# Optimization experiments

Hardware: AMD Instinct MI355X
Metric: run time of the kernel (lower is better)

The kernel has to match this reference:

```python
import jax, jax.numpy as jnp
import numpy as np

H = 512

def setup_inputs() -> dict:
    key = jax.random.key(0)
    ks = jax.random.split(key, 8)
    b, s, m, n, h = 8, 128, 32, 64, H
    sc = 1.0 / np.sqrt(h)
    return {
        "x": jax.random.normal(ks[0], (b, s, m, h), dtype=jnp.float32),
        "y": jax.random.normal(ks[1], (b, s, n, h), dtype=jnp.float32),
        # MultiHeadSelfAtt (additive self-attentive pooling: b*m*h -> b*h)
        "Wa1": jax.random.normal(ks[2], (h, h), dtype=jnp.float32) * sc,
        "ba1": jnp.zeros((h,), dtype=jnp.float32),
        "wa2": jax.random.normal(ks[3], (h,), dtype=jnp.float32) * sc,
        # gate Linear(2h -> h), torch layout weight: (h, 2h)
        "Wl": jax.random.normal(ks[4], (h, 2 * h), dtype=jnp.float32) * (1.0 / np.sqrt(2 * h)),
        "bl": jnp.zeros((h,), dtype=jnp.float32),
    }

def reference(x, y, Wa1, ba1, wa2, Wl, bl):
    h = x.shape[-1]
    # attentive pooling over m for every (b, s) slice: b s m h -> b s h
    scores = jnp.tanh(x @ Wa1 + ba1) @ wa2          # b s m
    attn = jax.nn.softmax(scores, axis=-1)
    pooled = jnp.einsum('bsm,bsmh->bsh', attn, x)   # b s h
    # step i (i>=1) uses pooled x at step i-1
    i_x = pooled[:, :-1]                            # b (s-1) h
    Wy, Wi = Wl[:, :h], Wl[:, h:]                   # split concat-linear
    pre = jnp.einsum('bsnh,gh->bsng', y[:, 1:], Wy) \
        + (i_x @ Wi.T + bl)[:, :, None, :]          # b (s-1) n h
    gate = jax.nn.sigmoid(pre)
    out_rest = y[:, 1:] + i_x[:, :, None, :] * gate
    return jnp.concatenate([y[:, :1], out_rest], axis=1)  # b s n h
```

## Files before the change

kernel.cpp:

```cpp
#include <hip/hip_runtime.h>
#include <cstdint>
#include <cstddef>

#define H 512
#define SEQ 128

typedef __bf16 v8bf __attribute__((ext_vector_type(8)));
typedef float v4f __attribute__((ext_vector_type(4)));
typedef unsigned short v8us __attribute__((ext_vector_type(8)));

__device__ __forceinline__ unsigned short f2bf(float f) {
    unsigned int u = __float_as_uint(f);
    u = (u + 0x7FFFu + ((u >> 16) & 1u)) >> 16;
    return (unsigned short)u;
}
__device__ __forceinline__ float bf2f(unsigned short h) {
    return __uint_as_float(((unsigned int)h) << 16);
}
__device__ __forceinline__ v8bf load_bf8(const unsigned short* p) {
    return *reinterpret_cast<const v8bf*>(p);
}
__device__ __forceinline__ float fast_tanh(float v) {
    float e = __expf(2.f * v);
    return 1.f - 2.f * __builtin_amdgcn_rcpf(e + 1.f);
}
__device__ __forceinline__ float fast_sigmoid(float v) {
    return __builtin_amdgcn_rcpf(1.f + __expf(-v));
}
__device__ __forceinline__ v8us cvt8u(float4 lo, float4 hi) {
    v8us r;
    r[0] = f2bf(lo.x); r[1] = f2bf(lo.y); r[2] = f2bf(lo.z); r[3] = f2bf(lo.w);
    r[4] = f2bf(hi.x); r[5] = f2bf(hi.y); r[6] = f2bf(hi.z); r[7] = f2bf(hi.w);
    return r;
}


__global__ __launch_bounds__(256) void prep_kernel(
        const float* __restrict__ Wa1, const float* __restrict__ Wl,
        unsigned short* __restrict__ WyS, unsigned short* __restrict__ WiS,
        unsigned short* __restrict__ WaS) {
    int tg = blockIdx.x * 256 + threadIdx.x;
    int mat = tg >> 15;
    int idx = tg & 32767;
    int lane = idx & 63;
    int ks = (idx >> 6) & 15;
    int c = idx >> 10;
    int g = c * 16 + (lane & 15);
    int hb = ks * 32 + ((lane >> 4) << 3);
    unsigned short o[8];
    unsigned short* dst;
    if (mat == 0) {
        const float* s = Wl + (size_t)g * 1024 + hb;
#pragma unroll
        for (int j = 0; j < 8; ++j) o[j] = f2bf(s[j]);
        dst = WyS + (size_t)idx * 8;
    } else if (mat == 1) {
        const float* s = Wl + (size_t)g * 1024 + 512 + hb;
#pragma unroll
        for (int j = 0; j < 8; ++j) o[j] = f2bf(s[j]);
        dst = WiS + (size_t)idx * 8;
    } else {
#pragma unroll
        for (int j = 0; j < 8; ++j) o[j] = f2bf(Wa1[(size_t)(hb + j) * H + g]);
        dst = WaS + (size_t)idx * 8;
    }
    *reinterpret_cast<ushort4*>(dst)     = *reinterpret_cast<ushort4*>(&o[0]);
    *reinterpret_cast<ushort4*>(dst + 4) = *reinterpret_cast<ushort4*>(&o[4]);
}

__global__ __launch_bounds__(256, 4) void attn_pool_kernel(
        const float* __restrict__ x, const unsigned short* __restrict__ WaS,
        const float* __restrict__ ba1, const float* __restrict__ wa2,
        float* __restrict__ ixf, unsigned short* __restrict__ ixb) {
    __shared__ __align__(16) unsigned short Xb[32][520];
    __shared__ float attn[32];
    __shared__ float scpart[4][32];

    int bid = blockIdx.x;
    int b = bid / 127, s = bid % 127;
    int t = threadIdx.x;

    const float4* x4 = reinterpret_cast<const float4*>(x + (size_t)(b * SEQ + s) * 32 * H);
#pragma unroll
    for (int i = 0; i < 16; ++i) {
        int idx4 = t + i * 256;
        float4 v = x4[idx4];
        int e = idx4 * 4, m = e >> 9, h = e & 511;
        ushort4 o;
        o.x = f2bf(v.x); o.y = f2bf(v.y); o.z = f2bf(v.z); o.w = f2bf(v.w);
        *reinterpret_cast<ushort4*>(&Xb[m][h]) = o;
    }
    __syncthreads();

    int w = t >> 6, lane = t & 63, q = lane >> 4, c16 = lane & 15;

    v4f acc[2][8];
#pragma unroll
    for (int mi = 0; mi < 2; ++mi)
#pragma unroll
        for (int ci = 0; ci < 8; ++ci) acc[mi][ci] = (v4f){0.f, 0.f, 0.f, 0.f};

    const unsigned short* Bb = WaS + (size_t)(w * 8 * 16) * 512 + lane * 8;

#pragma unroll
    for (int ks = 0; ks < 16; ++ks) {
        v8bf a0 = load_bf8(&Xb[c16][ks * 32 + q * 8]);
        v8bf a1 = load_bf8(&Xb[16 + c16][ks * 32 + q * 8]);
#pragma unroll
        for (int ci = 0; ci < 8; ++ci) {
            v8bf bb = load_bf8(Bb + (size_t)(ci * 16 + ks) * 512);
            acc[0][ci] = __builtin_amdgcn_mfma_f32_16x16x32_bf16(a0, bb, acc[0][ci], 0, 0, 0);
            acc[1][ci] = __builtin_amdgcn_mfma_f32_16x16x32_bf16(a1, bb, acc[1][ci], 0, 0, 0);
        }
    }

    float sr[2][4] = {{0.f, 0.f, 0.f, 0.f}, {0.f, 0.f, 0.f, 0.f}};
#pragma unroll
    for (int ci = 0; ci < 8; ++ci) {
        int g = (w * 8 + ci) * 16 + c16;
        float w2 = wa2[g];
        float bv = ba1[g];
#pragma unroll
        for (int mi = 0; mi < 2; ++mi)
#pragma unroll
            for (int i = 0; i < 4; ++i)
                sr[mi][i] += w2 * fast_tanh(acc[mi][ci][i] + bv);
    }
#pragma unroll
    for (int off = 1; off < 16; off <<= 1) {
#pragma unroll
        for (int mi = 0; mi < 2; ++mi)
#pragma unroll
            for (int i = 0; i < 4; ++i) sr[mi][i] += __shfl_xor(sr[mi][i], off);
    }
    if (c16 == 0) {
#pragma unroll
        for (int mi = 0; mi < 2; ++mi)
#pragma unroll
            for (int i = 0; i < 4; ++i) scpart[w][mi * 16 + q * 4 + i] = sr[mi][i];
    }
    __syncthreads();

    if (t < 64) {
        int m = t & 31;
        float v = scpart[0][m] + scpart[1][m] + scpart[2][m] + scpart[3][m];
        float mx = v;
#pragma unroll
        for (int off = 1; off < 32; off <<= 1) mx = fmaxf(mx, __shfl_xor(mx, off));
        float e = __expf(v - mx);
        float sum = e;
#pragma unroll
        for (int off = 1; off < 32; off <<= 1) sum += __shfl_xor(sum, off);
        if (t < 32) attn[m] = e * __builtin_amdgcn_rcpf(sum);
    }
    __syncthreads();

    int h0 = t * 2;
    float p0 = 0.f, p1 = 0.f;
#pragma unroll
    for (int m = 0; m < 32; ++m) {
        float am = attn[m];
        p0 += am * bf2f(Xb[m][h0]);
        p1 += am * bf2f(Xb[m][h0 + 1]);
    }
    size_t r = (size_t)bid;
    ixf[r * H + h0] = p0;
    ixf[r * H + h0 + 1] = p1;
    ixb[r * H + h0] = f2bf(p0);
    ixb[r * H + h0 + 1] = f2bf(p1);
}

__global__ __launch_bounds__(256) void ipre_kernel(
        const unsigned short* __restrict__ ixb, const unsigned short* __restrict__ WiS,
        const float* __restrict__ bl, float* __restrict__ ipre) {
    int row16 = blockIdx.x * 16;
    int t = threadIdx.x, w = t >> 6, lane = t & 63, q = lane >> 4, c16 = lane & 15;
    int c0 = blockIdx.y * 8 + w * 2;

    v4f acc0 = {0.f, 0.f, 0.f, 0.f};
    v4f acc1 = {0.f, 0.f, 0.f, 0.f};
    const unsigned short* arow = ixb + (size_t)(row16 + c16) * H + q * 8;
#pragma unroll
    for (int ks = 0; ks < 16; ++ks) {
        v8bf a = load_bf8(arow + ks * 32);
        acc0 = __builtin_amdgcn_mfma_f32_16x16x32_bf16(
            a, load_bf8(WiS + (size_t)(c0 * 16 + ks) * 512 + lane * 8), acc0, 0, 0, 0);
        acc1 = __builtin_amdgcn_mfma_f32_16x16x32_bf16(
            a, load_bf8(WiS + (size_t)((c0 + 1) * 16 + ks) * 512 + lane * 8), acc1, 0, 0, 0);
    }
#pragma unroll
    for (int cc = 0; cc < 2; ++cc) {
        int g = (c0 + cc) * 16 + c16;
        float blv = bl[g];
        v4f a = cc ? acc1 : acc0;
#pragma unroll
        for (int i = 0; i < 4; ++i) {
            int row = row16 + q * 4 + i;
            if (row < 1016) ipre[(size_t)row * H + g] = a[i] + blv;
        }
    }
}

__global__ __launch_bounds__(512, 4) void main_kernel(
        const float* __restrict__ y, const unsigned short* __restrict__ WyS,
        const float* __restrict__ ixf, const float* __restrict__ ipre,
        float* __restrict__ out) {
    int bid = blockIdx.x;
    int t = threadIdx.x;

    if (bid >= 1016) {
        int cb = bid - 1016;
        int b = cb >> 1, half = cb & 1;
        size_t base = ((size_t)(b * SEQ)) * 64 * H + (size_t)half * 32 * H;
        const float4* y4 = reinterpret_cast<const float4*>(y + base);
        float4* o4 = reinterpret_cast<float4*>(out + base);
#pragma unroll
        for (int i = 0; i < 8; ++i) o4[t + i * 512] = y4[t + i * 512];
        return;
    }

    int rg = bid >> 1;
    int ch = bid & 1;

    __shared__ __align__(16) char arena[57344];
    unsigned short* Ab = (unsigned short*)arena;
    unsigned short* Bbuf = (unsigned short*)(arena + 20480);
    float* ip_s = (float*)(arena + 53248);
    float* ix_s = (float*)(arena + 55296);
    float* ep   = (float*)arena;

    int t0 = rg * 2;

    int arow  = t >> 2;
    int acol0 = (t & 3) * 8;
    int atid  = t0 + (arow >> 6);
    int ab    = atid / 127, asm1 = atid % 127;
    const float* yrow = y + ((size_t)(ab * SEQ + asm1 + 1) * 64 + (arow & 63)) * H;

    int w = t >> 6, lane = t & 63, q = lane >> 4, c16 = lane & 15;
    int ck0 = w * 2;
    const unsigned short* bsrc0 = WyS + (size_t)((ch * 16 + ck0) * 16) * 512 + lane * 8;
    const unsigned short* bsrc1 = WyS + (size_t)((ch * 16 + ck0 + 1) * 16) * 512 + lane * 8;

    {
        int tile = t >> 8, gl = t & 255;
        size_t rrow = (size_t)(t0 + tile) * H + ch * 256 + gl;
        ip_s[t] = ipre[rrow];
        ix_s[t] = ixf[rrow];
    }

    {
        float4 a0 = *reinterpret_cast<const float4*>(yrow + acol0);
        float4 a1 = *reinterpret_cast<const float4*>(yrow + acol0 + 4);
        v8us b0 = *reinterpret_cast<const v8us*>(bsrc0);
        v8us b1 = *reinterpret_cast<const v8us*>(bsrc1);
        *reinterpret_cast<v8us*>(&Ab[arow * 40 + acol0]) = cvt8u(a0, a1);
        *reinterpret_cast<v8us*>(&Bbuf[ck0 * 512 + lane * 8]) = b0;
        *reinterpret_cast<v8us*>(&Bbuf[(ck0 + 1) * 512 + lane * 8]) = b1;
    }
    __syncthreads();

    int wr = w >> 1;
    int wc = w & 1;

    v4f acc[2][8];
#pragma unroll
    for (int rt = 0; rt < 2; ++rt)
#pragma unroll
        for (int ci = 0; ci < 8; ++ci) acc[rt][ci] = (v4f){0.f, 0.f, 0.f, 0.f};

#pragma unroll
    for (int p = 0; p < 16; ++p) {
        const int cur = p & 1;
        float4 na0, na1; v8us nb0, nb1;
        if (p < 15) {
            na0 = *reinterpret_cast<const float4*>(yrow + (p + 1) * 32 + acol0);
            na1 = *reinterpret_cast<const float4*>(yrow + (p + 1) * 32 + acol0 + 4);
            nb0 = *reinterpret_cast<const v8us*>(bsrc0 + (p + 1) * 512);
            nb1 = *reinterpret_cast<const v8us*>(bsrc1 + (p + 1) * 512);
        }

        v8bf af0 = load_bf8(&Ab[cur * 5120 + (wr * 32 + c16) * 40 + q * 8]);
        v8bf af1 = load_bf8(&Ab[cur * 5120 + (wr * 32 + 16 + c16) * 40 + q * 8]);
#pragma unroll
        for (int ci = 0; ci < 8; ++ci) {
            v8bf bf = load_bf8(&Bbuf[cur * 8192 + (wc * 8 + ci) * 512 + lane * 8]);
            acc[0][ci] = __builtin_amdgcn_mfma_f32_16x16x32_bf16(af0, bf, acc[0][ci], 0, 0, 0);
            acc[1][ci] = __builtin_amdgcn_mfma_f32_16x16x32_bf16(af1, bf, acc[1][ci], 0, 0, 0);
        }

        if (p < 15) {
            *reinterpret_cast<v8us*>(&Ab[(cur ^ 1) * 5120 + arow * 40 + acol0]) = cvt8u(na0, na1);
            *reinterpret_cast<v8us*>(&Bbuf[(cur ^ 1) * 8192 + ck0 * 512 + lane * 8]) = nb0;
            *reinterpret_cast<v8us*>(&Bbuf[(cur ^ 1) * 8192 + (ck0 + 1) * 512 + lane * 8]) = nb1;
            __syncthreads();
        }
    }

    int tile = wr >> 1;
    size_t obase0 = ((size_t)((t0 / 127) * SEQ + t0 % 127 + 1) * 64) * H;
    size_t obase1 = ((size_t)(((t0 + 1) / 127) * SEQ + (t0 + 1) % 127 + 1) * 64) * H;

#pragma unroll
    for (int slab = 0; slab < 4; ++slab) {
        __syncthreads();
        if (wr == slab) {
#pragma unroll
            for (int ci = 0; ci < 8; ++ci) {
                int gl = wc * 128 + ci * 16 + c16;
                float ip = ip_s[tile * 256 + gl];
                float ixv = ix_s[tile * 256 + gl];
#pragma unroll
                for (int rt = 0; rt < 2; ++rt)
#pragma unroll
                    for (int i = 0; i < 4; ++i) {
                        int rl = rt * 16 + q * 4 + i;
                        ep[rl * 260 + gl] = ixv * fast_sigmoid(acc[rt][ci][i] + ip);
                    }
            }
        }
        __syncthreads();
#pragma unroll
        for (int k = 0; k < 4; ++k) {
            int c = t + k * 512;
            int rl = c >> 6;
            int cx = (c & 63) * 4;
            int browg = slab * 32 + rl;
            int tl = browg >> 6;
            int n = browg & 63;
            size_t off = (tl ? obase1 : obase0) + (size_t)n * H + ch * 256 + cx;
            float4 g4 = *reinterpret_cast<const float4*>(&ep[rl * 260 + cx]);
            float4 y4 = *reinterpret_cast<const float4*>(&y[off]);
            float4 o;
            o.x = y4.x + g4.x; o.y = y4.y + g4.y;
            o.z = y4.z + g4.z; o.w = y4.w + g4.w;
            *reinterpret_cast<float4*>(&out[off]) = o;
        }
    }
}

extern "C" void kernel_launch(void* const* d_in, const int* in_sizes, int n_in,
                              void* d_out, int out_size, void* d_ws, size_t ws_size,
                              hipStream_t stream) {
    const float* x   = (const float*)d_in[0];
    const float* y   = (const float*)d_in[1];
    const float* Wa1 = (const float*)d_in[2];
    const float* ba1 = (const float*)d_in[3];
    const float* wa2 = (const float*)d_in[4];
    const float* Wl  = (const float*)d_in[5];
    const float* bl  = (const float*)d_in[6];
    float* out = (float*)d_out;

    char* ws = (char*)d_ws;
    unsigned short* WyS  = (unsigned short*)(ws);
    unsigned short* WiS  = (unsigned short*)(ws + 524288);
    unsigned short* WaS  = (unsigned short*)(ws + 1048576);
    float*          ixf  = (float*)(ws + 1572864);
    unsigned short* ixb  = (unsigned short*)(ws + 3670016);
    float*          ipre = (float*)(ws + 4718592);

    hipLaunchKernelGGL(prep_kernel, dim3(384), dim3(256), 0, stream, Wa1, Wl, WyS, WiS, WaS);
    hipLaunchKernelGGL(attn_pool_kernel, dim3(1016), dim3(256), 0, stream,
                       x, WaS, ba1, wa2, ixf, ixb);
    hipLaunchKernelGGL(ipre_kernel, dim3(64, 4), dim3(256), 0, stream, ixb, WiS, bl, ipre);
    hipLaunchKernelGGL(main_kernel, dim3(1032), dim3(512), 0, stream,
                       y, WyS, ixf, ipre, out);
}
```

Before: 150.9 us.

## Shrink main GEMM tile to one timestep, async-load weights into LDS, swizzle blocks

Restructures the main gated GEMM so each 256-thread block handles one (b,s) slice of 64 rows instead of two, doubling the grid to 2048 blocks and cutting LDS use. Weight tiles now go straight from global memory into LDS with global_load_lds, and the y activations are prefetched two stages ahead in registers so loads overlap the MFMA loop better. Block IDs are remapped with an XCD-style swizzle to improve L2 locality. The aim is more blocks resident per CU and better latency hiding, at the cost of each block reusing its weight tile across fewer rows, so weight traffic per output increases.

```diff
diff --git a/kernel.cpp b/kernel.cpp
--- a/kernel.cpp
+++ b/kernel.cpp
@@ -32,6 +32,11 @@
     r[0] = f2bf(lo.x); r[1] = f2bf(lo.y); r[2] = f2bf(lo.z); r[3] = f2bf(lo.w);
     r[4] = f2bf(hi.x); r[5] = f2bf(hi.y); r[6] = f2bf(hi.z); r[7] = f2bf(hi.w);
     return r;
+}
+__device__ __forceinline__ void gll16(const unsigned short* g, unsigned short* l) {
+    __builtin_amdgcn_global_load_lds(
+        (const __attribute__((address_space(1))) unsigned int*)g,
+        (__attribute__((address_space(3))) unsigned int*)l, 16, 0, 0);
 }
 
 
@@ -201,68 +206,64 @@
     }
 }
 
-__global__ __launch_bounds__(512, 4) void main_kernel(
+__global__ __launch_bounds__(256, 3) void main_kernel(
         const float* __restrict__ y, const unsigned short* __restrict__ WyS,
         const float* __restrict__ ixf, const float* __restrict__ ipre,
         float* __restrict__ out) {
-    int bid = blockIdx.x;
+    int bid0 = blockIdx.x;
     int t = threadIdx.x;
 
-    if (bid >= 1016) {
-        int cb = bid - 1016;
+    if (bid0 >= 2032) {
+        int cb = bid0 - 2032;
         int b = cb >> 1, half = cb & 1;
         size_t base = ((size_t)(b * SEQ)) * 64 * H + (size_t)half * 32 * H;
         const float4* y4 = reinterpret_cast<const float4*>(y + base);
         float4* o4 = reinterpret_cast<float4*>(out + base);
 #pragma unroll
-        for (int i = 0; i < 8; ++i) o4[t + i * 512] = y4[t + i * 512];
+        for (int i = 0; i < 16; ++i) o4[t + i * 256] = y4[t + i * 256];
         return;
     }
 
+    int bid = (bid0 & 7) * 254 + (bid0 >> 3);
     int rg = bid >> 1;
     int ch = bid & 1;
 
-    __shared__ __align__(16) char arena[57344];
-    unsigned short* Ab = (unsigned short*)arena;
-    unsigned short* Bbuf = (unsigned short*)(arena + 20480);
-    float* ip_s = (float*)(arena + 53248);
-    float* ix_s = (float*)(arena + 55296);
+    __shared__ __align__(16) char arena[45056];
+    unsigned short* As = (unsigned short*)arena;
+    unsigned short* Bs = (unsigned short*)(arena + 10240);
+    float* ip_s = (float*)(arena + 43008);
+    float* ix_s = (float*)(arena + 44032);
     float* ep   = (float*)arena;
 
-    int t0 = rg * 2;
-
-    int arow  = t >> 2;
-    int acol0 = (t & 3) * 8;
-    int atid  = t0 + (arow >> 6);
-    int ab    = atid / 127, asm1 = atid % 127;
-    const float* yrow = y + ((size_t)(ab * SEQ + asm1 + 1) * 64 + (arow & 63)) * H;
+    int b0 = rg / 127, s0 = rg % 127;
+    size_t obase = ((size_t)(b0 * SEQ + s0 + 1) * 64) * H;
 
     int w = t >> 6, lane = t & 63, q = lane >> 4, c16 = lane & 15;
-    int ck0 = w * 2;
-    const unsigned short* bsrc0 = WyS + (size_t)((ch * 16 + ck0) * 16) * 512 + lane * 8;
-    const unsigned short* bsrc1 = WyS + (size_t)((ch * 16 + ck0 + 1) * 16) * 512 + lane * 8;
+    int wr = w >> 1, wc = w & 1;
+
+    int arow = t >> 2;
+    int acol = (t & 3) * 8;
+    const float* ysrc = y + obase + (size_t)arow * H + acol;
+
+    const unsigned short* bbase = WyS + ((size_t)((ch * 16 + w * 4) * 16)) * 512 + lane * 8;
 
     {
-        int tile = t >> 8, gl = t & 255;
-        size_t rrow = (size_t)(t0 + tile) * H + ch * 256 + gl;
-        ip_s[t] = ipre[rrow];
-        ix_s[t] = ixf[rrow];
-    }
-
-    {
-        float4 a0 = *reinterpret_cast<const float4*>(yrow + acol0);
-        float4 a1 = *reinterpret_cast<const float4*>(yrow + acol0 + 4);
-        v8us b0 = *reinterpret_cast<const v8us*>(bsrc0);
-        v8us b1 = *reinterpret_cast<const v8us*>(bsrc1);
-        *reinterpret_cast<v8us*>(&Ab[arow * 40 + acol0]) = cvt8u(a0, a1);
-        *reinterpret_cast<v8us*>(&Bbuf[ck0 * 512 + lane * 8]) = b0;
-        *reinterpret_cast<v8us*>(&Bbuf[(ck0 + 1) * 512 + lane * 8]) = b1;
-    }
+        size_t rr = (size_t)rg * H + ch * 256 + t;
+        ip_s[t] = ipre[rr];
+        ix_s[t] = ixf[rr];
+    }
+
+#pragma unroll
+    for (int j = 0; j < 4; ++j)
+        gll16(bbase + (size_t)j * 8192, &Bs[(w * 4 + j) * 512]);
+    float4 alo[2], ahi[2];
+    alo[0] = *reinterpret_cast<const float4*>(ysrc);
+    ahi[0] = *reinterpret_cast<const float4*>(ysrc + 4);
+    alo[1] = *reinterpret_cast<const float4*>(ysrc + 32);
+    ahi[1] = *reinterpret_cast<const float4*>(ysrc + 36);
+    *reinterpret_cast<v8us*>(&As[arow * 40 + acol]) = cvt8u(alo[0], ahi[0]);
     __syncthreads();
 
-    int wr = w >> 1;
-    int wc = w & 1;
-
     v4f acc[2][8];
 #pragma unroll
     for (int rt = 0; rt < 2; ++rt)
@@ -271,69 +272,66 @@
 
 #pragma unroll
     for (int p = 0; p < 16; ++p) {
-        const int cur = p & 1;
-        float4 na0, na1; v8us nb0, nb1;
+        const int buf = p & 1;
+        const int nxt = buf ^ 1;
         if (p < 15) {
-            na0 = *reinterpret_cast<const float4*>(yrow + (p + 1) * 32 + acol0);
-            na1 = *reinterpret_cast<const float4*>(yrow + (p + 1) * 32 + acol0 + 4);
-            nb0 = *reinterpret_cast<const v8us*>(bsrc0 + (p + 1) * 512);
-            nb1 = *reinterpret_cast<const v8us*>(bsrc1 + (p + 1) * 512);
-        }
-
-        v8bf af0 = load_bf8(&Ab[cur * 5120 + (wr * 32 + c16) * 40 + q * 8]);
-        v8bf af1 = load_bf8(&Ab[cur * 5120 + (wr * 32 + 16 + c16) * 40 + q * 8]);
+#pragma unroll
+            for (int j = 0; j < 4; ++j)
+                gll16(bbase + (size_t)j * 8192 + (size_t)(p + 1) * 512,
+                      &Bs[nxt * 8192 + (w * 4 + j) * 512]);
+        }
+        if (p < 14) {
+            alo[buf] = *reinterpret_cast<const float4*>(ysrc + (p + 2) * 32);
+            ahi[buf] = *reinterpret_cast<const float4*>(ysrc + (p + 2) * 32 + 4);
+        }
+        if (p < 15) {
+            *reinterpret_cast<v8us*>(&As[nxt * 2560 + arow * 40 + acol]) =
+                cvt8u(alo[nxt], ahi[nxt]);
+        }
+
+        v8bf af0 = load_bf8(&As[buf * 2560 + (wr * 32 + c16) * 40 + q * 8]);
+        v8bf af1 = load_bf8(&As[buf * 2560 + (wr * 32 + 16 + c16) * 40 + q * 8]);
 #pragma unroll
         for (int ci = 0; ci < 8; ++ci) {
-            v8bf bf = load_bf8(&Bbuf[cur * 8192 + (wc * 8 + ci) * 512 + lane * 8]);
-            acc[0][ci] = __builtin_amdgcn_mfma_f32_16x16x32_bf16(af0, bf, acc[0][ci], 0, 0, 0);
-            acc[1][ci] = __builtin_amdgcn_mfma_f32_16x16x32_bf16(af1, bf, acc[1][ci], 0, 0, 0);
-        }
-
-        if (p < 15) {
-            *reinterpret_cast<v8us*>(&Ab[(cur ^ 1) * 5120 + arow * 40 + acol0]) = cvt8u(na0, na1);
-            *reinterpret_cast<v8us*>(&Bbuf[(cur ^ 1) * 8192 + ck0 * 512 + lane * 8]) = nb0;
-            *reinterpret_cast<v8us*>(&Bbuf[(cur ^ 1) * 8192 + (ck0 + 1) * 512 + lane * 8]) = nb1;
-            __syncthreads();
-        }
-    }
-
-    int tile = wr >> 1;
-    size_t obase0 = ((size_t)((t0 / 127) * SEQ + t0 % 127 + 1) * 64) * H;
-    size_t obase1 = ((size_t)(((t0 + 1) / 127) * SEQ + (t0 + 1) % 127 + 1) * 64) * H;
-
-#pragma unroll
-    for (int slab = 0; slab < 4; ++slab) {
+            v8bf bfc = load_bf8(&Bs[buf * 8192 + (wc * 8 + ci) * 512 + lane * 8]);
+            acc[0][ci] = __builtin_amdgcn_mfma_f32_16x16x32_bf16(af0, bfc, acc[0][ci], 0, 0, 0);
+            acc[1][ci] = __builtin_amdgcn_mfma_f32_16x16x32_bf16(af1, bfc, acc[1][ci], 0, 0, 0);
+        }
+
+        if (p < 15) __syncthreads();
+    }
+
+#pragma unroll
+    for (int s = 0; s < 2; ++s) {
         __syncthreads();
-        if (wr == slab) {
+        if (wr == s) {
 #pragma unroll
             for (int ci = 0; ci < 8; ++ci) {
                 int gl = wc * 128 + ci * 16 + c16;
-                float ip = ip_s[tile * 256 + gl];
-                float ixv = ix_s[tile * 256 + gl];
+                float ipv = ip_s[gl];
+                float ixv = ix_s[gl];
 #pragma unroll
                 for (int rt = 0; rt < 2; ++rt)
 #pragma unroll
                     for (int i = 0; i < 4; ++i) {
                         int rl = rt * 16 + q * 4 + i;
-                        ep[rl * 260 + gl] = ixv * fast_sigmoid(acc[rt][ci][i] + ip);
+                        ep[rl * 260 + gl] = ixv * fast_sigmoid(acc[rt][ci][i] + ipv);
                     }
             }
         }
         __syncthreads();
 #pragma unroll
-        for (int k = 0; k < 4; ++k) {
-            int c = t + k * 512;
+        for (int k = 0; k < 8; ++k) {
+            int c = t + k * 256;
             int rl = c >> 6;
             int cx = (c & 63) * 4;
-            int browg = slab * 32 + rl;
-            int tl = browg >> 6;
-            int n = browg & 63;
-            size_t off = (tl ? obase1 : obase0) + (size_t)n * H + ch * 256 + cx;
+            int n = s * 32 + rl;
+            size_t off = obase + (size_t)n * H + ch * 256 + cx;
             float4 g4 = *reinterpret_cast<const float4*>(&ep[rl * 260 + cx]);
-            float4 y4 = *reinterpret_cast<const float4*>(&y[off]);
+            float4 yv = *reinterpret_cast<const float4*>(&y[off]);
             float4 o;
-            o.x = y4.x + g4.x; o.y = y4.y + g4.y;
-            o.z = y4.z + g4.z; o.w = y4.w + g4.w;
+            o.x = yv.x + g4.x; o.y = yv.y + g4.y;
+            o.z = yv.z + g4.z; o.w = yv.w + g4.w;
             *reinterpret_cast<float4*>(&out[off]) = o;
         }
     }
@@ -363,6 +361,6 @@
     hipLaunchKernelGGL(attn_pool_kernel, dim3(1016), dim3(256), 0, stream,
                        x, WaS, ba1, wa2, ixf, ixb);
     hipLaunchKernelGGL(ipre_kernel, dim3(64, 4), dim3(256), 0, stream, ixb, WiS, bl, ipre);
-    hipLaunchKernelGGL(main_kernel, dim3(1032), dim3(512), 0, stream,
+    hipLaunchKernelGGL(main_kernel, dim3(2048), dim3(256), 0, stream,
                        y, WyS, ixf, ipre, out);
 }
```

After: 152.2 us. Within noise of the previous version (+0.9%).

## Prefetch two K-steps ahead in registers and remap block order for XCD locality

Applied to the files above, without the earlier changes.

The GEMM main loop now keeps global loads for the y and Wy tiles two iterations ahead in double-buffered registers. It writes the next stage to shared memory before the MFMAs rather than after, so memory latency can hide behind more compute. Block IDs for the compute blocks are also permuted as (bid&7)*127+(bid>>3), so that consecutive row groups land on the same XCD and can share L2. The cost is higher register pressure from the extra prefetch buffers, under a launch bound of 4 blocks of 512 threads.

```diff
diff --git a/kernel.cpp b/kernel.cpp
--- a/kernel.cpp
+++ b/kernel.cpp
@@ -205,11 +205,11 @@
         const float* __restrict__ y, const unsigned short* __restrict__ WyS,
         const float* __restrict__ ixf, const float* __restrict__ ipre,
         float* __restrict__ out) {
-    int bid = blockIdx.x;
+    int bid0 = blockIdx.x;
     int t = threadIdx.x;
 
-    if (bid >= 1016) {
-        int cb = bid - 1016;
+    if (bid0 >= 1016) {
+        int cb = bid0 - 1016;
         int b = cb >> 1, half = cb & 1;
         size_t base = ((size_t)(b * SEQ)) * 64 * H + (size_t)half * 32 * H;
         const float4* y4 = reinterpret_cast<const float4*>(y + base);
@@ -218,6 +218,8 @@
         for (int i = 0; i < 8; ++i) o4[t + i * 512] = y4[t + i * 512];
         return;
     }
+
+    int bid = (bid0 & 7) * 127 + (bid0 >> 3);
 
     int rg = bid >> 1;
     int ch = bid & 1;
@@ -249,11 +251,17 @@
         ix_s[t] = ixf[rrow];
     }
 
+    float4 a_lo[2], a_hi[2]; v8us b0r[2], b1r[2];
+
     {
         float4 a0 = *reinterpret_cast<const float4*>(yrow + acol0);
         float4 a1 = *reinterpret_cast<const float4*>(yrow + acol0 + 4);
         v8us b0 = *reinterpret_cast<const v8us*>(bsrc0);
         v8us b1 = *reinterpret_cast<const v8us*>(bsrc1);
+        a_lo[1] = *reinterpret_cast<const float4*>(yrow + 32 + acol0);
+        a_hi[1] = *reinterpret_cast<const float4*>(yrow + 32 + acol0 + 4);
+        b0r[1] = *reinterpret_cast<const v8us*>(bsrc0 + 512);
+        b1r[1] = *reinterpret_cast<const v8us*>(bsrc1 + 512);
         *reinterpret_cast<v8us*>(&Ab[arow * 40 + acol0]) = cvt8u(a0, a1);
         *reinterpret_cast<v8us*>(&Bbuf[ck0 * 512 + lane * 8]) = b0;
         *reinterpret_cast<v8us*>(&Bbuf[(ck0 + 1) * 512 + lane * 8]) = b1;
@@ -272,12 +280,18 @@
 #pragma unroll
     for (int p = 0; p < 16; ++p) {
         const int cur = p & 1;
-        float4 na0, na1; v8us nb0, nb1;
+        const int nxt = cur ^ 1;
+        if (p < 14) {
+            a_lo[cur] = *reinterpret_cast<const float4*>(yrow + (p + 2) * 32 + acol0);
+            a_hi[cur] = *reinterpret_cast<const float4*>(yrow + (p + 2) * 32 + acol0 + 4);
+            b0r[cur] = *reinterpret_cast<const v8us*>(bsrc0 + (p + 2) * 512);
+            b1r[cur] = *reinterpret_cast<const v8us*>(bsrc1 + (p + 2) * 512);
+        }
         if (p < 15) {
-            na0 = *reinterpret_cast<const float4*>(yrow + (p + 1) * 32 + acol0);
-            na1 = *reinterpret_cast<const float4*>(yrow + (p + 1) * 32 + acol0 + 4);
-            nb0 = *reinterpret_cast<const v8us*>(bsrc0 + (p + 1) * 512);
-            nb1 = *reinterpret_cast<const v8us*>(bsrc1 + (p + 1) * 512);
+            *reinterpret_cast<v8us*>(&Ab[nxt * 5120 + arow * 40 + acol0]) =
+                cvt8u(a_lo[nxt], a_hi[nxt]);
+            *reinterpret_cast<v8us*>(&Bbuf[nxt * 8192 + ck0 * 512 + lane * 8]) = b0r[nxt];
+            *reinterpret_cast<v8us*>(&Bbuf[nxt * 8192 + (ck0 + 1) * 512 + lane * 8]) = b1r[nxt];
         }
 
         v8bf af0 = load_bf8(&Ab[cur * 5120 + (wr * 32 + c16) * 40 + q * 8]);
@@ -289,12 +303,7 @@
             acc[1][ci] = __builtin_amdgcn_mfma_f32_16x16x32_bf16(af1, bf, acc[1][ci], 0, 0, 0);
         }
 
-        if (p < 15) {
-            *reinterpret_cast<v8us*>(&Ab[(cur ^ 1) * 5120 + arow * 40 + acol0]) = cvt8u(na0, na1);
-            *reinterpret_cast<v8us*>(&Bbuf[(cur ^ 1) * 8192 + ck0 * 512 + lane * 8]) = nb0;
-            *reinterpret_cast<v8us*>(&Bbuf[(cur ^ 1) * 8192 + (ck0 + 1) * 512 + lane * 8]) = nb1;
-            __syncthreads();
-        }
+        if (p < 15) __syncthreads();
     }
 
     int tile = wr >> 1;
```

Result: faster. 146.4 us, median of 3 (-3.0%).
